# Kernel tuning notes

Measured on AMD Instinct MI355X. Metric: run time of the kernel, lower is better.

Reference implementation:

```python
import jax, jax.numpy as jnp
import numpy as np

N = 4096      # num_nodes
D_IN = 768    # input_dim
HID = 512     # hidden_dim per head
D_OUT = 768   # output_dim
H = 4         # num_heads
ALPHA = 0.2   # LeakyReLU slope
NEG_BIG = -9e15


def _layer_norm(x, g, b, eps=1e-5):
    m = jnp.mean(x, axis=-1, keepdims=True)
    v = jnp.var(x, axis=-1, keepdims=True)
    return (x - m) * jax.lax.rsqrt(v + eps) * g + b


def _multihead_gat(h, mask, ew, W, a, concat):
    # h: [N, F_in], W: [H, F_in, O], a: [H, 2*O], mask/ew: [N, N]
    O = W.shape[-1]
    Wh = jnp.einsum('nf,hfo->hno', h, W)                      # [H, N, O]
    # e[h,i,j] = leakyrelu(a1.Wh[i] + a2.Wh[j]) -- equivalent to the
    # concat(Wh_i, Wh_j) @ a formulation, without the O(N^2 * 2O) tensor.
    s_src = jnp.einsum('hno,ho->hn', Wh, a[:, :O])            # [H, N]
    s_dst = jnp.einsum('hno,ho->hn', Wh, a[:, O:])            # [H, N]
    e = jax.nn.leaky_relu(s_src[:, :, None] + s_dst[:, None, :], negative_slope=ALPHA)
    att = jnp.where(mask[None], e, NEG_BIG)
    if ew is not None:
        att = att * ew[None]                                   # faithful: scale AFTER masking
    att = jax.nn.softmax(att, axis=-1)                         # dropout is identity at eval
    hp = jnp.einsum('hnm,hmo->hno', att, Wh)                   # [H, N, O]
    if concat:
        return jax.nn.elu(jnp.transpose(hp, (1, 0, 2)).reshape(h.shape[0], H * O))
    return jnp.mean(hp, axis=0)                                # concat=False: mean, no ELU


def setup_inputs() -> dict:
    key = jax.random.key(0)
    ks = jax.random.split(key, 10)
    return {
        'node_features': jax.random.normal(ks[0], (N, D_IN), jnp.float32),
        'adjacency': jax.random.randint(ks[1], (N, N), 0, 2, jnp.int32),
        'edge_weights': jax.random.uniform(ks[2], (N, N), jnp.float32),
        'W0': (jax.random.normal(ks[3], (H, D_IN, HID)) * 0.05).astype(jnp.float32),
        'a0': (jax.random.normal(ks[4], (H, 2 * HID)) * 0.05).astype(jnp.float32),
        'W1': (jax.random.normal(ks[5], (H, HID * H, D_OUT)) * 0.02).astype(jnp.float32),
        'a1': (jax.random.normal(ks[6], (H, 2 * D_OUT)) * 0.05).astype(jnp.float32),
        'rp0_w': (jax.random.normal(ks[7], (D_IN, HID * H)) * 0.02).astype(jnp.float32),
        'rp0_b': jnp.zeros((HID * H,), jnp.float32),
        'rp1_w': (jax.random.normal(ks[8], (HID * H, D_OUT)) * 0.02).astype(jnp.float32),
        'rp1_b': jnp.zeros((D_OUT,), jnp.float32),
        'ln0_g': jnp.ones((HID * H,), jnp.float32),
        'ln0_b': jnp.zeros((HID * H,), jnp.float32),
        'ln1_g': jnp.ones((D_OUT,), jnp.float32),
        'ln1_b': jnp.zeros((D_OUT,), jnp.float32),
    }


def reference(node_features, adjacency, edge_weights, W0, a0, W1, a1,
              rp0_w, rp0_b, rp1_w, rp1_b, ln0_g, ln0_b, ln1_g, ln1_b):
    n = node_features.shape[0]
    adj = adjacency.astype(jnp.float32) + jnp.eye(n, dtype=jnp.float32)  # add self-loops
    mask = adj > 0
    h = node_features
    # layer 0: concat heads -> [N, H*HID], residual projection, LN, ELU (dropout=identity)
    h1 = _multihead_gat(h, mask, edge_weights, W0, a0, concat=True)
    h1 = h1 + (h @ rp0_w + rp0_b)
    h1 = _layer_norm(h1, ln0_g, ln0_b)
    h1 = jax.nn.elu(h1)
    # layer 1 (last): mean over heads -> [N, D_OUT], residual projection, LN
    h2 = _multihead_gat(h1, mask, edge_weights, W1, a1, concat=False)
    h2 = h2 + (h1 @ rp1_w + rp1_b)
    h2 = _layer_norm(h2, ln1_g, ln1_b)
    return h2
```

## Files before the change

### kernel.cpp

```cpp
#include <hip/hip_runtime.h>


typedef unsigned short u16;
typedef unsigned char u8;
typedef unsigned long long u64;
using short8  = __attribute__((ext_vector_type(8))) short;
using float4v = __attribute__((ext_vector_type(4))) float;
using int4v   = __attribute__((ext_vector_type(4))) int;
using int8v   = __attribute__((ext_vector_type(8))) int;

#define NN 4096
#define NHEADS 4

__device__ __forceinline__ u16 f2bf(float f) {
  union { float f; unsigned u; } v; v.f = f;
  unsigned u = v.u;
  return (u16)((u + 0x7FFFu + ((u >> 16) & 1u)) >> 16);
}
__device__ __forceinline__ float bf2f(u16 x) {
  union { unsigned u; float f; } v; v.u = ((unsigned)x) << 16; return v.f;
}
__device__ __forceinline__ unsigned pk_fp8x4(float a, float b, float c, float d) {
  int lo = __builtin_amdgcn_cvt_pk_fp8_f32(a, b, 0, false);
  return (unsigned)__builtin_amdgcn_cvt_pk_fp8_f32(c, d, lo, true);
}

__device__ __forceinline__ void async16(const void* g, void* l) {
  __builtin_amdgcn_global_load_lds(
      (const __attribute__((address_space(1))) unsigned int*)g,
      (__attribute__((address_space(3))) unsigned int*)l, 16, 0, 0);
}

__global__ __launch_bounds__(256) void cast_f32_bf16(const float* __restrict__ in,
                                                     u16* __restrict__ out, int n) {
  int i = blockIdx.x * 256 + threadIdx.x;
  if (i < n) out[i] = f2bf(in[i]);
}

__global__ __launch_bounds__(256) void adj2bits(const int* __restrict__ adj,
                                                u64* __restrict__ bits) {
  size_t gw = (size_t)blockIdx.x * 4 + (threadIdx.x >> 6);
  int lane = threadIdx.x & 63;
  int v = adj[gw * 64 + lane];
  u64 b = __ballot(v != 0);
  if (lane == 0) bits[gw] = b;
}

__global__ __launch_bounds__(256) void transcast_f32(const float* __restrict__ in,
                                                     u16* __restrict__ out, int R, int C) {
  __shared__ float t[32][33];
  size_t zoff = (size_t)blockIdx.z * R * C;
  in += zoff; out += zoff;
  int c0 = blockIdx.x * 32, r0 = blockIdx.y * 32;
  int tx = threadIdx.x & 31, ty = threadIdx.x >> 5;
#pragma unroll
  for (int i = 0; i < 32; i += 8)
    t[ty + i][tx] = in[(size_t)(r0 + ty + i) * C + (c0 + tx)];
  __syncthreads();
#pragma unroll
  for (int i = 0; i < 32; i += 8)
    out[(size_t)(c0 + ty + i) * R + (r0 + tx)] = f2bf(t[tx][ty + i]);
}

__global__ __launch_bounds__(256) void wa_kernel(const float* __restrict__ W,
                                                 const float* __restrict__ a,
                                                 float* __restrict__ wa, int F, int O) {
  int gw = blockIdx.x * 4 + (threadIdx.x >> 6);
  int lane = threadIdx.x & 63;
  int total = 2 * NHEADS * F;
  if (gw >= total) return;
  int side = gw / (NHEADS * F);
  int rem = gw - side * NHEADS * F;
  int h = rem / F, f = rem - h * F;
  const float* wrow = W + ((size_t)h * F + f) * O;
  const float* av = a + (size_t)h * 2 * O + (size_t)side * O;
  float s = 0.f;
  for (int o = lane; o < O; o += 64) s += wrow[o] * av[o];
#pragma unroll
  for (int off = 32; off > 0; off >>= 1) s += __shfl_down(s, off);
  if (lane == 0) wa[gw] = s;
}

__global__ __launch_bounds__(256) void s8_kernel_f32(const float* __restrict__ X,
                                                     const float* __restrict__ wa,
                                                     float* __restrict__ sout, int F) {
  int n = blockIdx.x * 4 + (threadIdx.x >> 6);
  int lane = threadIdx.x & 63;
  const float* x = X + (size_t)n * F;
  float acc[8] = {};
  for (int f = lane; f < F; f += 64) {
    float xv = x[f];
#pragma unroll
    for (int k = 0; k < 8; k++) acc[k] += xv * wa[(size_t)k * F + f];
  }
#pragma unroll
  for (int k = 0; k < 8; k++) {
    float s = acc[k];
#pragma unroll
    for (int off = 32; off > 0; off >>= 1) s += __shfl_down(s, off);
    if (lane == 0) sout[(size_t)k * NN + n] = s;
  }
}

__global__ __launch_bounds__(256) void s8_kernel_bf16(const u16* __restrict__ X,
                                                      const float* __restrict__ wa,
                                                      float* __restrict__ sout, int F) {
  int n = blockIdx.x * 4 + (threadIdx.x >> 6);
  int lane = threadIdx.x & 63;
  const u16* x = X + (size_t)n * F;
  float acc[8] = {};
  for (int f = lane; f < F; f += 64) {
    float xv = bf2f(x[f]);
#pragma unroll
    for (int k = 0; k < 8; k++) acc[k] += xv * wa[(size_t)k * F + f];
  }
#pragma unroll
  for (int k = 0; k < 8; k++) {
    float s = acc[k];
#pragma unroll
    for (int off = 32; off > 0; off >>= 1) s += __shfl_down(s, off);
    if (lane == 0) sout[(size_t)k * NN + n] = s;
  }
}

__global__ __launch_bounds__(256) void sdmax_kernel(const float* __restrict__ s,
                                                    float* __restrict__ out) {
  int h = blockIdx.x, tid = threadIdx.x;
  const float* sd = s + (size_t)(NHEADS + h) * NN;
  float m = -3e38f;
  for (int i = tid; i < NN; i += 256) m = fmaxf(m, sd[i]);
  __shared__ float red[4];
#pragma unroll
  for (int off = 32; off > 0; off >>= 1) m = fmaxf(m, __shfl_down(m, off));
  if ((tid & 63) == 0) red[tid >> 6] = m;
  __syncthreads();
  if (tid == 0) out[h] = fmaxf(fmaxf(red[0], red[1]), fmaxf(red[2], red[3]));
}

template <int G>
__global__ __launch_bounds__(256) void pexp_g_kernel(const u64* __restrict__ mb,
                                                     const float* __restrict__ ew,
                                                     const float* __restrict__ s,
                                                     const float* __restrict__ sdmax,
                                                     u8* __restrict__ P,
                                                     float* __restrict__ L, int hb) {
  __shared__ u64 mrow[64];
  __shared__ float lred[G][4];
  int i = blockIdx.x, tid = threadIdx.x;
  if (tid < 64) mrow[tid] = mb[(size_t)i * 64 + tid];
  float sr[G], mp[G], lacc[G];
#pragma unroll
  for (int z = 0; z < G; z++) {
    sr[z] = s[(size_t)(hb + z) * NN + i];
    mp[z] = fmaxf(0.0f, sr[z] + sdmax[hb + z]);
    lacc[z] = 0.f;
  }
  const float4* wrow = (const float4*)(ew + (size_t)i * NN);
  __syncthreads();
  for (int jv = tid; jv < NN / 4; jv += 256) {
    float4 w = wrow[jv];
    int j0 = jv * 4;
    u64 mw = mrow[jv >> 4] >> (j0 & 63);
    float we[4]; we[0] = w.x; we[1] = w.y; we[2] = w.z; we[3] = w.w;
    bool m[4];
#pragma unroll
    for (int k = 0; k < 4; k++) m[k] = ((mw >> k) & 1ull) || (j0 + k == i);
#pragma unroll
    for (int z = 0; z < G; z++) {
      const float4 sd4 = *(const float4*)(s + (size_t)(NHEADS + hb + z) * NN + j0);
      float sd[4]; sd[0] = sd4.x; sd[1] = sd4.y; sd[2] = sd4.z; sd[3] = sd4.w;
      float p[4];
#pragma unroll
      for (int k = 0; k < 4; k++) {
        float x = sr[z] + sd[k];
        float e = x > 0.f ? x : 0.2f * x;
        float v = (m[k] ? e : -9e15f) * we[k];
        p[k] = __expf(v - mp[z]);
        lacc[z] += p[k];
      }
      *(unsigned*)(P + ((size_t)z * NN + i) * NN + j0) = pk_fp8x4(p[0], p[1], p[2], p[3]);
    }
  }
#pragma unroll
  for (int z = 0; z < G; z++) {
    float r = lacc[z];
#pragma unroll
    for (int off = 32; off > 0; off >>= 1) r += __shfl_down(r, off);
    if ((tid & 63) == 0) lred[z][tid >> 6] = r;
  }
  __syncthreads();
  if (tid < G)
    L[(size_t)(hb + tid) * NN + i] = lred[tid][0] + lred[tid][1] + lred[tid][2] + lred[tid][3];
}

__global__ __launch_bounds__(256) void gemm_proj(const u16* __restrict__ A,
                                                 const u16* __restrict__ Bt,
                                                 u8* __restrict__ F8T,
                                                 float* __restrict__ F32,
                                                 const float* __restrict__ bias,
                                                 int K, int split, int ldcF) {
  int row0 = blockIdx.x * 128;
  int col0 = blockIdx.y * 128;

  __shared__ u16 ldsA[2][128 * 64];
  __shared__ u16 ldsB[2][128 * 64];

  int tid = threadIdx.x;
  int wave = tid >> 6, lane = tid & 63;
  int wm = wave >> 1, wn = wave & 1;
  int lm = lane & 15, quad = lane >> 4;

  int sr = tid >> 3, sc = tid & 7;
  int scg = sc ^ (sr & 7);
  const u16* aPtr = A  + (size_t)(row0 + sr) * K + scg * 8;
  const u16* bPtr = Bt + (size_t)(col0 + sr) * K + scg * 8;
  const size_t rowStep = (size_t)32 * K;

  float4v acc[4][4] = {};

  auto stage = [&](int buf, int k0) {
    u16* la = &ldsA[buf][wave * 512];
    u16* lb = &ldsB[buf][wave * 512];
#pragma unroll
    for (int b = 0; b < 4; b++) {
      async16(aPtr + k0 + b * rowStep, la + b * 2048);
      async16(bPtr + k0 + b * rowStep, lb + b * 2048);
    }
  };

  const int nt = K >> 6;
  stage(0, 0);
  stage(1, 64);
  asm volatile("s_waitcnt vmcnt(8)" ::: "memory");
  __builtin_amdgcn_s_barrier();
  __builtin_amdgcn_sched_barrier(0);

  for (int t = 0; t < nt; t++) {
    int cur = t & 1;
    const u16* LA = ldsA[cur];
    const u16* LB = ldsB[cur];
    short8 af[4][2], bf[4][2];
#pragma unroll
    for (int s = 0; s < 4; s++) {
      int ra = wm * 64 + s * 16 + lm;
      int rb = wn * 64 + s * 16 + lm;
      int swa = ra & 7, swb = rb & 7;
      af[s][0] = *(const short8*)(&LA[ra * 64 + ((quad ^ swa) * 8)]);
      af[s][1] = *(const short8*)(&LA[ra * 64 + (((4 + quad) ^ swa) * 8)]);
      bf[s][0] = *(const short8*)(&LB[rb * 64 + ((quad ^ swb) * 8)]);
      bf[s][1] = *(const short8*)(&LB[rb * 64 + (((4 + quad) ^ swb) * 8)]);
    }
#pragma unroll
    for (int i = 0; i < 4; i++)
#pragma unroll
      for (int j = 0; j < 4; j++) {
        acc[i][j] = __builtin_amdgcn_mfma_f32_16x16x32_bf16(af[i][0], bf[j][0], acc[i][j], 0, 0, 0);
        acc[i][j] = __builtin_amdgcn_mfma_f32_16x16x32_bf16(af[i][1], bf[j][1], acc[i][j], 0, 0, 0);
      }
    __builtin_amdgcn_s_barrier();
    __builtin_amdgcn_sched_barrier(0);
    if (t + 2 < nt) {
      stage(cur, (t + 2) << 6);
      asm volatile("s_waitcnt vmcnt(8)" ::: "memory");
    } else {
      asm volatile("s_waitcnt vmcnt(0)" ::: "memory");
    }
    __builtin_amdgcn_s_barrier();
    __builtin_amdgcn_sched_barrier(0);
  }

  if (col0 < split) {
#pragma unroll
    for (int i = 0; i < 4; i++) {
#pragma unroll
      for (int j = 0; j < 4; j++) {
        int grow0 = row0 + wm * 64 + i * 16 + (lane >> 4) * 4;
        int gcol = col0 + wn * 64 + j * 16 + lm;
        unsigned pk = pk_fp8x4(acc[i][j][0], acc[i][j][1], acc[i][j][2], acc[i][j][3]);
        *(unsigned*)&F8T[(size_t)gcol * NN + grow0] = pk;
      }
    }
  } else {
#pragma unroll
    for (int i = 0; i < 4; i++) {
#pragma unroll
      for (int j = 0; j < 4; j++) {
#pragma unroll
        for (int r = 0; r < 4; r++) {
          int grow = row0 + wm * 64 + i * 16 + (lane >> 4) * 4 + r;
          int gcol = col0 + wn * 64 + j * 16 + lm - split;
          F32[(size_t)grow * ldcF + gcol] = acc[i][j][r] + bias[gcol];
        }
      }
    }
  }
}

template <int MODE>
__global__ __launch_bounds__(256) void gemm_mx(const u8* __restrict__ A,
                                               const u8* __restrict__ Bt,
                                               float* __restrict__ Cout,
                                               int ldc, int coloff_base, int coloff_step,
                                               size_t bStride, size_t cStride) {
  constexpr int K = NN;
  int h = blockIdx.z;
  const u8* Ab = A + (size_t)h * ((size_t)NN * NN);
  const u8* Bb = Bt + (size_t)h * bStride;
  int row0 = blockIdx.x * 128;
  int col0 = blockIdx.y * 128;
  int coloff = coloff_base + h * coloff_step;

  __shared__ u8 ldsA[2][128 * 128];
  __shared__ u8 ldsB[2][128 * 128];

  int tid = threadIdx.x;
  int wave = tid >> 6, lane = tid & 63;
  int wm = wave >> 1, wn = wave & 1;
  int lm = lane & 15, quad = lane >> 4;

  int sr = tid >> 3, sc = tid & 7;
  int scg = sc ^ (sr & 7);
  const u8* aPtr = Ab + (size_t)(row0 + sr) * K + scg * 16;
  const u8* bPtr = Bb + (size_t)(col0 + sr) * K + scg * 16;
  const size_t rowStep = (size_t)32 * K;

  float4v acc[4][4] = {};

  auto stage = [&](int buf, int k0) {
    u8* la = &ldsA[buf][wave * 1024];
    u8* lb = &ldsB[buf][wave * 1024];
#pragma unroll
    for (int b = 0; b < 4; b++) {
      async16(aPtr + k0 + b * rowStep, la + b * 4096);
      async16(bPtr + k0 + b * rowStep, lb + b * 4096);
    }
  };

  const int nt = K >> 7;
  stage(0, 0);
  stage(1, 128);
  asm volatile("s_waitcnt vmcnt(8)" ::: "memory");
  __builtin_amdgcn_s_barrier();
  __builtin_amdgcn_sched_barrier(0);

  for (int t = 0; t < nt; t++) {
    int cur = t & 1;
    const u8* LA = ldsA[cur];
    const u8* LB = ldsB[cur];
    int8v a32[4], b32[4];
#pragma unroll
    for (int s = 0; s < 4; s++) {
      int ra = wm * 64 + s * 16 + lm;
      int rb = wn * 64 + s * 16 + lm;
      int swa = ra & 7, swb = rb & 7;
      int4v alo = *(const int4v*)(&LA[ra * 128 + (((2 * quad) ^ swa) * 16)]);
      int4v ahi = *(const int4v*)(&LA[ra * 128 + (((2 * quad + 1) ^ swa) * 16)]);
      int4v blo = *(const int4v*)(&LB[rb * 128 + (((2 * quad) ^ swb) * 16)]);
      int4v bhi = *(const int4v*)(&LB[rb * 128 + (((2 * quad + 1) ^ swb) * 16)]);
      a32[s][0] = alo[0]; a32[s][1] = alo[1]; a32[s][2] = alo[2]; a32[s][3] = alo[3];
      a32[s][4] = ahi[0]; a32[s][5] = ahi[1]; a32[s][6] = ahi[2]; a32[s][7] = ahi[3];
      b32[s][0] = blo[0]; b32[s][1] = blo[1]; b32[s][2] = blo[2]; b32[s][3] = blo[3];
      b32[s][4] = bhi[0]; b32[s][5] = bhi[1]; b32[s][6] = bhi[2]; b32[s][7] = bhi[3];
    }
#pragma unroll
    for (int i = 0; i < 4; i++)
#pragma unroll
      for (int j = 0; j < 4; j++)
        acc[i][j] = __builtin_amdgcn_mfma_scale_f32_16x16x128_f8f6f4(
            a32[i], b32[j], acc[i][j], 0, 0, 0, 127, 0, 127);
    __builtin_amdgcn_s_barrier();
    __builtin_amdgcn_sched_barrier(0);
    if (t + 2 < nt) {
      stage(cur, (t + 2) << 7);
      asm volatile("s_waitcnt vmcnt(8)" ::: "memory");
    } else {
      asm volatile("s_waitcnt vmcnt(0)" ::: "memory");
    }
    __builtin_amdgcn_s_barrier();
    __builtin_amdgcn_sched_barrier(0);
  }

#pragma unroll
  for (int i = 0; i < 4; i++) {
#pragma unroll
    for (int j = 0; j < 4; j++) {
#pragma unroll
      for (int r = 0; r < 4; r++) {
        int grow = row0 + wm * 64 + i * 16 + quad * 4 + r;
        int gcol = col0 + wn * 64 + j * 16 + lm;
        float v = acc[i][j][r];
        if constexpr (MODE == 2) {
          Cout[(size_t)grow * ldc + coloff + gcol] = v;
        } else {
          Cout[(size_t)h * cStride + (size_t)grow * ldc + gcol] = v;
        }
      }
    }
  }
}

__global__ __launch_bounds__(256) void ln0_kernel(const float* __restrict__ accin,
                                                  const float* __restrict__ rp,
                                                  const float* __restrict__ Lsum,
                                                  const float* __restrict__ g,
                                                  const float* __restrict__ b,
                                                  u16* __restrict__ h1b) {
  const int C = 2048;
  int n = blockIdx.x, tid = threadIdx.x;
  __shared__ float xs[2048];
  __shared__ float red[2][4];
  __shared__ float mrs[2];
  float linv[NHEADS];
#pragma unroll
  for (int h = 0; h < NHEADS; h++) linv[h] = 1.0f / Lsum[(size_t)h * NN + n];
  float sum = 0.f, sq = 0.f;
  const float* ar = accin + (size_t)n * C;
  const float* rr = rp + (size_t)n * C;
  for (int c = tid; c < C; c += 256) {
    float v = ar[c] * linv[c >> 9];
    v = v > 0.f ? v : (__expf(v) - 1.f);
    float x = v + rr[c];
    xs[c] = x; sum += x; sq += x * x;
  }
#pragma unroll
  for (int off = 32; off > 0; off >>= 1) { sum += __shfl_down(sum, off); sq += __shfl_down(sq, off); }
  if ((tid & 63) == 0) { red[0][tid >> 6] = sum; red[1][tid >> 6] = sq; }
  __syncthreads();
  if (tid == 0) {
    float s = red[0][0] + red[0][1] + red[0][2] + red[0][3];
    float q = red[1][0] + red[1][1] + red[1][2] + red[1][3];
    float mean = s / C, var = q / C - mean * mean;
    mrs[0] = mean; mrs[1] = rsqrtf(var + 1e-5f);
  }
  __syncthreads();
  float mean = mrs[0], rstd = mrs[1];
  for (int c = tid; c < C; c += 256) {
    float y = (xs[c] - mean) * rstd * g[c] + b[c];
    float z = y > 0.f ? y : (__expf(y) - 1.f);
    h1b[(size_t)n * C + c] = f2bf(z);
  }
}

__global__ __launch_bounds__(256) void ln1_kernel(const float* __restrict__ hp1,
                                                  const float* __restrict__ rp1,
                                                  const float* __restrict__ Lsum,
                                                  const float* __restrict__ g,
                                                  const float* __restrict__ b,
                                                  float* __restrict__ out) {
  const int C = 768;
  int n = blockIdx.x, tid = threadIdx.x;
  __shared__ float xs[768];
  __shared__ float red[2][4];
  __shared__ float mrs[2];
  float linv[NHEADS];
#pragma unroll
  for (int h = 0; h < NHEADS; h++) linv[h] = 0.25f / Lsum[(size_t)h * NN + n];
  float sum = 0.f, sq = 0.f;
  for (int c = tid; c < C; c += 256) {
    float x = hp1[((size_t)0 * NN + n) * C + c] * linv[0] +
              hp1[((size_t)1 * NN + n) * C + c] * linv[1] +
              hp1[((size_t)2 * NN + n) * C + c] * linv[2] +
              hp1[((size_t)3 * NN + n) * C + c] * linv[3];
    x += rp1[(size_t)n * C + c];
    xs[c] = x; sum += x; sq += x * x;
  }
#pragma unroll
  for (int off = 32; off > 0; off >>= 1) { sum += __shfl_down(sum, off); sq += __shfl_down(sq, off); }
  if ((tid & 63) == 0) { red[0][tid >> 6] = sum; red[1][tid >> 6] = sq; }
  __syncthreads();
  if (tid == 0) {
    float s = red[0][0] + red[0][1] + red[0][2] + red[0][3];
    float q = red[1][0] + red[1][1] + red[1][2] + red[1][3];
    float mean = s / C, var = q / C - mean * mean;
    mrs[0] = mean; mrs[1] = rsqrtf(var + 1e-5f);
  }
  __syncthreads();
  float mean = mrs[0], rstd = mrs[1];
  for (int c = tid; c < C; c += 256)
    out[(size_t)n * C + c] = (xs[c] - mean) * rstd * g[c] + b[c];
}

extern "C" void kernel_launch(void* const* d_in, const int* in_sizes, int n_in,
                              void* d_out, int out_size, void* d_ws, size_t ws_size,
                              hipStream_t stream) {
  (void)in_sizes; (void)n_in; (void)out_size;
  const float* X    = (const float*)d_in[0];
  const int*   adj  = (const int*)d_in[1];
  const float* ew   = (const float*)d_in[2];
  const float* W0   = (const float*)d_in[3];
  const float* a0   = (const float*)d_in[4];
  const float* W1   = (const float*)d_in[5];
  const float* a1   = (const float*)d_in[6];
  const float* rp0w = (const float*)d_in[7];
  const float* rp0b = (const float*)d_in[8];
  const float* rp1w = (const float*)d_in[9];
  const float* rp1b = (const float*)d_in[10];
  const float* ln0g = (const float*)d_in[11];
  const float* ln0b = (const float*)d_in[12];
  const float* ln1g = (const float*)d_in[13];
  const float* ln1b = (const float*)d_in[14];
  float* out = (float*)d_out;
  char* wsb = (char*)d_ws;

  constexpr size_t OFF_XBF   = 0;
  constexpr size_t OFF_W0T   = 6291456;
  constexpr size_t OFF_RP0WT = 9437184;
  constexpr size_t OFF_W1T   = 12582912;
  constexpr size_t OFF_RP1WT = 25165824;
  constexpr size_t OFF_WA0   = 28311552;
  constexpr size_t OFF_WA1   = 28336128;
  constexpr size_t OFF_S0    = 28401664;
  constexpr size_t OFF_S1    = 28532736;
  constexpr size_t OFF_L0    = 28664320;
  constexpr size_t OFF_L1    = 28729856;
  constexpr size_t OFF_H1B   = 28795392;
  constexpr size_t D         = 45572608;
  constexpr size_t PD        = D + 50331648;
  constexpr size_t PN        = (size_t)NN * NN;
  constexpr size_t OFF_HP1   = PD + 4 * PN;
  constexpr size_t OFF_MASK  = 213344768;
  constexpr size_t OFF_SM0   = 215441920;
  constexpr size_t OFF_SM1   = 215442176;

  u16*   XBF   = (u16*)(wsb + OFF_XBF);
  u16*   W0T   = (u16*)(wsb + OFF_W0T);
  u16*   RP0WT = (u16*)(wsb + OFF_RP0WT);
  u16*   W1T   = (u16*)(wsb + OFF_W1T);
  u16*   RP1WT = (u16*)(wsb + OFF_RP1WT);
  float* WA0   = (float*)(wsb + OFF_WA0);
  float* WA1   = (float*)(wsb + OFF_WA1);
  float* S0    = (float*)(wsb + OFF_S0);
  float* S1    = (float*)(wsb + OFF_S1);
  float* L0    = (float*)(wsb + OFF_L0);
  float* L1    = (float*)(wsb + OFF_L1);
  u16*   H1B   = (u16*)(wsb + OFF_H1B);
  u8*    WH0T  = (u8*)(wsb + D);
  float* RP0   = (float*)(wsb + D + 16777216);
  u8*    WH1T  = (u8*)(wsb + D);
  float* RP1   = (float*)(wsb + D + 25165824);
  u8*    P     = (u8*)(wsb + PD);
  float* HP1   = (float*)(wsb + OFF_HP1);
  float* ACC0  = (float*)(wsb + OFF_HP1);
  u64*   MASK  = (u64*)(wsb + OFF_MASK);
  float* SM0   = (float*)(wsb + OFF_SM0);
  float* SM1   = (float*)(wsb + OFF_SM1);

  const int G = (ws_size >= OFF_HP1 + 50331648) ? 4 : 1;

  adj2bits<<<dim3(65536), 256, 0, stream>>>(adj, MASK);
  cast_f32_bf16<<<dim3((NN * 768 + 255) / 256), 256, 0, stream>>>(X, XBF, NN * 768);
  transcast_f32<<<dim3(16, 24, 4), 256, 0, stream>>>(W0, W0T, 768, 512);
  transcast_f32<<<dim3(24, 64, 4), 256, 0, stream>>>(W1, W1T, 2048, 768);
  transcast_f32<<<dim3(64, 24, 1), 256, 0, stream>>>(rp0w, RP0WT, 768, 2048);
  transcast_f32<<<dim3(24, 64, 1), 256, 0, stream>>>(rp1w, RP1WT, 2048, 768);

  wa_kernel<<<dim3(2 * NHEADS * 768 / 4), 256, 0, stream>>>(W0, a0, WA0, 768, 512);
  s8_kernel_f32<<<dim3(NN / 4), 256, 0, stream>>>(X, WA0, S0, 768);
  sdmax_kernel<<<dim3(NHEADS), 256, 0, stream>>>(S0, SM0);

  gemm_proj<<<dim3(32, 32), 256, 0, stream>>>(XBF, W0T, WH0T, RP0, rp0b, 768, 2048, 2048);

  for (int g = 0; g < NHEADS; g += G) {
    if (G == 4) pexp_g_kernel<4><<<dim3(NN), 256, 0, stream>>>(MASK, ew, S0, SM0, P, L0, g);
    else        pexp_g_kernel<1><<<dim3(NN), 256, 0, stream>>>(MASK, ew, S0, SM0, P, L0, g);
    gemm_mx<2><<<dim3(32, 4, G), 256, 0, stream>>>(P, WH0T + (size_t)g * 512 * NN,
        ACC0, 2048, g * 512, 512, (size_t)512 * NN, 0);
  }
  ln0_kernel<<<dim3(NN), 256, 0, stream>>>(ACC0, RP0, L0, ln0g, ln0b, H1B);

  wa_kernel<<<dim3(2 * NHEADS * 2048 / 4), 256, 0, stream>>>(W1, a1, WA1, 2048, 768);
  s8_kernel_bf16<<<dim3(NN / 4), 256, 0, stream>>>(H1B, WA1, S1, 2048);
  sdmax_kernel<<<dim3(NHEADS), 256, 0, stream>>>(S1, SM1);

  gemm_proj<<<dim3(32, 30), 256, 0, stream>>>(H1B, W1T, WH1T, RP1, rp1b, 2048, 3072, 768);

  for (int g = 0; g < NHEADS; g += G) {
    if (G == 4) pexp_g_kernel<4><<<dim3(NN), 256, 0, stream>>>(MASK, ew, S1, SM1, P, L1, g);
    else        pexp_g_kernel<1><<<dim3(NN), 256, 0, stream>>>(MASK, ew, S1, SM1, P, L1, g);
    gemm_mx<3><<<dim3(32, 6, G), 256, 0, stream>>>(P, WH1T + (size_t)g * 768 * NN,
        HP1 + (size_t)g * NN * 768, 768, 0, 0, (size_t)768 * NN, (size_t)NN * 768);
  }
  ln1_kernel<<<dim3(NN), 256, 0, stream>>>(HP1, RP1, L1, ln1g, ln1b, out);
}
```

Before: 604.3 us.

## Restructure projection GEMM to 256x256 tiles with 8-wave ping-pong pipeline

```diff
diff --git a/kernel.cpp b/kernel.cpp
--- a/kernel.cpp
+++ b/kernel.cpp
@@ -193,108 +193,138 @@
     L[(size_t)(hb + tid) * NN + i] = lred[tid][0] + lred[tid][1] + lred[tid][2] + lred[tid][3];
 }
 
-__global__ __launch_bounds__(256) void gemm_proj(const u16* __restrict__ A,
-                                                 const u16* __restrict__ Bt,
-                                                 u8* __restrict__ F8T,
-                                                 float* __restrict__ F32,
-                                                 const float* __restrict__ bias,
-                                                 int K, int split, int ldcF) {
-  int row0 = blockIdx.x * 128;
-  int col0 = blockIdx.y * 128;
-
-  __shared__ u16 ldsA[2][128 * 64];
-  __shared__ u16 ldsB[2][128 * 64];
+#define PH(CUR, MH, NH, VMN, STAGE)                                              \
+  {                                                                              \
+    asm volatile("s_waitcnt vmcnt(" #VMN ")" ::: "memory");                      \
+    short8 af[4][2], bb[2][2];                                                   \
+    _Pragma("unroll") for (int mi = 0; mi < 4; mi++) {                           \
+      int lr = mi * 32 + wm16 + lm;                                              \
+      int sw = lr & 7;                                                           \
+      const u16* ap = &LA[CUR][MH][lr * 64];                                     \
+      af[mi][0] = *(const short8*)(ap + ((quad ^ sw) * 8));                      \
+      af[mi][1] = *(const short8*)(ap + (((4 + quad) ^ sw) * 8));                \
+    }                                                                            \
+    _Pragma("unroll") for (int ni = 0; ni < 2; ni++) {                           \
+      int lc = ni * 64 + wn16 + lm;                                              \
+      int sw = lc & 7;                                                           \
+      const u16* bp = &LB[CUR][NH][lc * 64];                                     \
+      bb[ni][0] = *(const short8*)(bp + ((quad ^ sw) * 8));                      \
+      bb[ni][1] = *(const short8*)(bp + (((4 + quad) ^ sw) * 8));                \
+    }                                                                            \
+    STAGE;                                                                       \
+    __builtin_amdgcn_s_barrier();                                                \
+    asm volatile("s_waitcnt lgkmcnt(0)" ::: "memory");                           \
+    __builtin_amdgcn_sched_barrier(0);                                           \
+    __builtin_amdgcn_s_setprio(1);                                               \
+    _Pragma("unroll") for (int mi = 0; mi < 4; mi++)                             \
+      _Pragma("unroll") for (int ni = 0; ni < 2; ni++) {                         \
+        acc[MH * 4 + mi][NH * 2 + ni] = __builtin_amdgcn_mfma_f32_16x16x32_bf16( \
+            af[mi][0], bb[ni][0], acc[MH * 4 + mi][NH * 2 + ni], 0, 0, 0);       \
+        acc[MH * 4 + mi][NH * 2 + ni] = __builtin_amdgcn_mfma_f32_16x16x32_bf16( \
+            af[mi][1], bb[ni][1], acc[MH * 4 + mi][NH * 2 + ni], 0, 0, 0);       \
+      }                                                                          \
+    __builtin_amdgcn_s_setprio(0);                                               \
+    __builtin_amdgcn_s_barrier();                                                \
+  }
+
+__global__ __launch_bounds__(512, 2) void gemm_proj(const u16* __restrict__ A,
+                                                    const u16* __restrict__ Bt,
+                                                    u8* __restrict__ F8T,
+                                                    float* __restrict__ F32,
+                                                    const float* __restrict__ bias,
+                                                    int K, int split, int ldcF) {
+  int lin = blockIdx.y * 16 + blockIdx.x;
+  int nwg = gridDim.y * 16;
+  int cpx = nwg >> 3;
+  int swz = (lin & 7) * cpx + (lin >> 3);
+  int row0 = (swz & 15) * 256;
+  int col0 = (swz >> 4) * 256;
+
+  __shared__ u16 LA[2][2][8192];
+  __shared__ u16 LB[2][2][8192];
 
   int tid = threadIdx.x;
   int wave = tid >> 6, lane = tid & 63;
-  int wm = wave >> 1, wn = wave & 1;
+  int wm = wave >> 2, wn = wave & 3;
+  int wm16 = wm * 16, wn16 = wn * 16;
   int lm = lane & 15, quad = lane >> 4;
 
-  int sr = tid >> 3, sc = tid & 7;
-  int scg = sc ^ (sr & 7);
-  const u16* aPtr = A  + (size_t)(row0 + sr) * K + scg * 8;
-  const u16* bPtr = Bt + (size_t)(col0 + sr) * K + scg * 8;
-  const size_t rowStep = (size_t)32 * K;
-
-  float4v acc[4][4] = {};
-
-  auto stage = [&](int buf, int k0) {
-    u16* la = &ldsA[buf][wave * 512];
-    u16* lb = &ldsB[buf][wave * 512];
-#pragma unroll
-    for (int b = 0; b < 4; b++) {
-      async16(aPtr + k0 + b * rowStep, la + b * 2048);
-      async16(bPtr + k0 + b * rowStep, lb + b * 2048);
-    }
+  int r0 = tid >> 3;
+  int cg = (tid & 7) ^ (r0 & 7);
+  const u16* aSrc = A + (size_t)(row0 + r0) * K + cg * 8;
+  const u16* bSrc = Bt + (size_t)(col0 + r0) * K + cg * 8;
+
+  auto stA = [&](int d, int h, int kt) {
+    const u16* p = aSrc + (size_t)h * 128 * K + (size_t)kt * 64;
+    async16(p, &LA[d][h][wave * 512]);
+    async16(p + (size_t)64 * K, &LA[d][h][4096 + wave * 512]);
   };
-
-  const int nt = K >> 6;
-  stage(0, 0);
-  stage(1, 64);
-  asm volatile("s_waitcnt vmcnt(8)" ::: "memory");
+  auto stB = [&](int d, int h, int kt) {
+    const u16* p = bSrc + (size_t)h * 128 * K + (size_t)kt * 64;
+    async16(p, &LB[d][h][wave * 512]);
+    async16(p + (size_t)64 * K, &LB[d][h][4096 + wave * 512]);
+  };
+
+  float4v acc[8][4] = {};
+
+  const int NT = K >> 6;
+  const int NI = NT >> 1;
+
+  stB(0, 0, 0); stA(0, 0, 0); stA(0, 1, 0); stB(0, 1, 0);
+  stB(1, 0, 1); stA(1, 0, 1);
+  asm volatile("s_waitcnt vmcnt(6)" ::: "memory");
   __builtin_amdgcn_s_barrier();
-  __builtin_amdgcn_sched_barrier(0);
-
-  for (int t = 0; t < nt; t++) {
-    int cur = t & 1;
-    const u16* LA = ldsA[cur];
-    const u16* LB = ldsB[cur];
-    short8 af[4][2], bf[4][2];
-#pragma unroll
-    for (int s = 0; s < 4; s++) {
-      int ra = wm * 64 + s * 16 + lm;
-      int rb = wn * 64 + s * 16 + lm;
-      int swa = ra & 7, swb = rb & 7;
-      af[s][0] = *(const short8*)(&LA[ra * 64 + ((quad ^ swa) * 8)]);
-      af[s][1] = *(const short8*)(&LA[ra * 64 + (((4 + quad) ^ swa) * 8)]);
-      bf[s][0] = *(const short8*)(&LB[rb * 64 + ((quad ^ swb) * 8)]);
-      bf[s][1] = *(const short8*)(&LB[rb * 64 + (((4 + quad) ^ swb) * 8)]);
-    }
-#pragma unroll
-    for (int i = 0; i < 4; i++)
-#pragma unroll
-      for (int j = 0; j < 4; j++) {
-        acc[i][j] = __builtin_amdgcn_mfma_f32_16x16x32_bf16(af[i][0], bf[j][0], acc[i][j], 0, 0, 0);
-        acc[i][j] = __builtin_amdgcn_mfma_f32_16x16x32_bf16(af[i][1], bf[j][1], acc[i][j], 0, 0, 0);
-      }
-    __builtin_amdgcn_s_barrier();
-    __builtin_amdgcn_sched_barrier(0);
-    if (t + 2 < nt) {
-      stage(cur, (t + 2) << 6);
-      asm volatile("s_waitcnt vmcnt(8)" ::: "memory");
-    } else {
-      asm volatile("s_waitcnt vmcnt(0)" ::: "memory");
-    }
-    __builtin_amdgcn_s_barrier();
-    __builtin_amdgcn_sched_barrier(0);
+
+  for (int i = 0; i < NI - 1; i++) {
+    int kt1 = 2 * i + 1, kt2 = 2 * i + 2, kt3 = 2 * i + 3;
+    PH(0, 0, 0, 6, stA(1, 1, kt1));
+    PH(0, 1, 0, 6, stB(1, 1, kt1));
+    PH(0, 0, 1, 6, stB(0, 0, kt2));
+    PH(0, 1, 1, 6, stA(0, 0, kt2));
+    PH(1, 0, 0, 6, stA(0, 1, kt2));
+    PH(1, 1, 0, 6, stB(0, 1, kt2));
+    PH(1, 0, 1, 6, stB(1, 0, kt3));
+    PH(1, 1, 1, 6, stA(1, 0, kt3));
+  }
+  {
+    int kt1 = NT - 1;
+    PH(0, 0, 0, 6, stA(1, 1, kt1));
+    PH(0, 1, 0, 6, stB(1, 1, kt1));
+    PH(0, 0, 1, 6, ((void)0));
+    PH(0, 1, 1, 4, ((void)0));
+    PH(1, 0, 0, 2, ((void)0));
+    PH(1, 1, 0, 0, ((void)0));
+    PH(1, 0, 1, 0, ((void)0));
+    PH(1, 1, 1, 0, ((void)0));
   }
 
   if (col0 < split) {
 #pragma unroll
-    for (int i = 0; i < 4; i++) {
-#pragma unroll
-      for (int j = 0; j < 4; j++) {
-        int grow0 = row0 + wm * 64 + i * 16 + (lane >> 4) * 4;
-        int gcol = col0 + wn * 64 + j * 16 + lm;
-        unsigned pk = pk_fp8x4(acc[i][j][0], acc[i][j][1], acc[i][j][2], acc[i][j][3]);
+    for (int m = 0; m < 8; m++) {
+#pragma unroll
+      for (int n = 0; n < 4; n++) {
+        int grow0 = row0 + m * 32 + wm16 + quad * 4;
+        int gcol = col0 + n * 64 + wn16 + lm;
+        unsigned pk = pk_fp8x4(acc[m][n][0], acc[m][n][1], acc[m][n][2], acc[m][n][3]);
         *(unsigned*)&F8T[(size_t)gcol * NN + grow0] = pk;
       }
     }
   } else {
 #pragma unroll
-    for (int i = 0; i < 4; i++) {
-#pragma unroll
-      for (int j = 0; j < 4; j++) {
+    for (int m = 0; m < 8; m++) {
+#pragma unroll
+      for (int n = 0; n < 4; n++) {
 #pragma unroll
         for (int r = 0; r < 4; r++) {
-          int grow = row0 + wm * 64 + i * 16 + (lane >> 4) * 4 + r;
-          int gcol = col0 + wn * 64 + j * 16 + lm - split;
-          F32[(size_t)grow * ldcF + gcol] = acc[i][j][r] + bias[gcol];
+          int grow = row0 + m * 32 + wm16 + quad * 4 + r;
+          int gcol = col0 + n * 64 + wn16 + lm - split;
+          F32[(size_t)grow * ldcF + gcol] = acc[m][n][r] + bias[gcol];
         }
       }
     }
   }
 }
+#undef PH
 
 template <int MODE>
 __global__ __launch_bounds__(256) void gemm_mx(const u8* __restrict__ A,
@@ -558,7 +588,7 @@
   s8_kernel_f32<<<dim3(NN / 4), 256, 0, stream>>>(X, WA0, S0, 768);
   sdmax_kernel<<<dim3(NHEADS), 256, 0, stream>>>(S0, SM0);
 
-  gemm_proj<<<dim3(32, 32), 256, 0, stream>>>(XBF, W0T, WH0T, RP0, rp0b, 768, 2048, 2048);
+  gemm_proj<<<dim3(16, 16), 512, 0, stream>>>(XBF, W0T, WH0T, RP0, rp0b, 768, 2048, 2048);
 
   for (int g = 0; g < NHEADS; g += G) {
     if (G == 4) pexp_g_kernel<4><<<dim3(NN), 256, 0, stream>>>(MASK, ew, S0, SM0, P, L0, g);
@@ -572,7 +602,7 @@
   s8_kernel_bf16<<<dim3(NN / 4), 256, 0, stream>>>(H1B, WA1, S1, 2048);
   sdmax_kernel<<<dim3(NHEADS), 256, 0, stream>>>(S1, SM1);
 
-  gemm_proj<<<dim3(32, 30), 256, 0, stream>>>(H1B, W1T, WH1T, RP1, rp1b, 2048, 3072, 768);
+  gemm_proj<<<dim3(16, 15), 512, 0, stream>>>(H1B, W1T, WH1T, RP1, rp1b, 2048, 3072, 768);
 
   for (int g = 0; g < NHEADS; g += G) {
     if (G == 4) pexp_g_kernel<4><<<dim3(NN), 256, 0, stream>>>(MASK, ew, S1, SM1, P, L1, g);
```

Result: no change. 608.3 us (+0.7%).
